# Kernel optimization log

Measured on AMD Instinct MI355X. Metric: run time of the kernel, lower is better.

## Reference

```python
import jax, jax.numpy as jnp
import numpy as np

D_E = 128
D_R = 128  # must equal D_E for the original torch code to typecheck
BN_EPS = 1e-5


def setup_inputs() -> dict:
    key = jax.random.key(0)
    ks = jax.random.split(key, 8)
    B, S = 16, 2048
    h = jax.random.normal(ks[0], (B, S, D_E), dtype=jnp.float32)
    r = jax.random.normal(ks[1], (B, S, D_R), dtype=jnp.float32)
    t = jax.random.normal(ks[2], (B, S, D_E), dtype=jnp.float32)
    # Xavier-uniform core tensor W: (d_r, d_e, d_e)
    limit = float(np.sqrt(6.0 / (D_R + D_E * D_E)))
    W = jax.random.uniform(ks[3], (D_R, D_E, D_E), minval=-limit, maxval=limit, dtype=jnp.float32)
    # BatchNorm1d params/buffers (inference mode)
    gamma0 = jnp.ones((D_E,), jnp.float32)
    beta0 = jnp.zeros((D_E,), jnp.float32)
    mean0 = 0.1 * jax.random.normal(ks[4], (D_E,), dtype=jnp.float32)
    var0 = jnp.abs(1.0 + 0.1 * jax.random.normal(ks[5], (D_E,), dtype=jnp.float32))
    gamma1 = jnp.ones((D_E,), jnp.float32)
    beta1 = jnp.zeros((D_E,), jnp.float32)
    mean1 = 0.1 * jax.random.normal(ks[6], (D_E,), dtype=jnp.float32)
    var1 = jnp.abs(1.0 + 0.1 * jax.random.normal(ks[7], (D_E,), dtype=jnp.float32))
    return {"h": h, "r": r, "t": t, "W": W,
            "gamma0": gamma0, "beta0": beta0, "mean0": mean0, "var0": var0,
            "gamma1": gamma1, "beta1": beta1, "mean1": mean1, "var1": var1}


def reference(h, r, t, W, gamma0, beta0, mean0, var0, gamma1, beta1, mean1, var1):
    B, S, D = h.shape  # D == d_e == d_r
    N = B * S
    # BatchNorm1d in eval mode over last dim; dropout is identity in eval.
    h_bn = (h - mean0) * jax.lax.rsqrt(var0 + BN_EPS) * gamma0 + beta0
    t_bn = (t - mean1) * jax.lax.rsqrt(var1 + BN_EPS) * gamma1 + beta1
    r2 = r.reshape(N, D)
    # torch.matmul((N,d_r), (d_r,d_e,d_e)) broadcasts -> shape (d_r, N, d_e):
    #   out[k, n, j] = sum_i r2[n, i] * W[k, i, j]
    # followed by .view(N, d_e, d_e) which reinterprets the flat buffer.
    W_mat = jnp.einsum('ni,kij->knj', r2, W).reshape(N, D, D)  # (N, d_e, d_e) after scrambled view
    # hr[n, j] = sum_d h_bn[n, d] * W_mat[n, d, j]
    hr = jnp.einsum('nd,ndj->nj', h_bn.reshape(N, D), W_mat)
    scores = jnp.sum(hr * t_bn.reshape(N, D), axis=-1)  # (N,)
    return scores.reshape(B, S)
```

## Files before the change

### kernel.cpp

```cpp
#include <hip/hip_runtime.h>


typedef __attribute__((ext_vector_type(8))) short bf16x8;
typedef __attribute__((ext_vector_type(4))) short s16x4;
typedef __attribute__((ext_vector_type(4))) float f32x4;

#define DPAD 136
#define BN_EPS 1e-5f

__device__ inline unsigned short f2bf(float f) {
  unsigned u = __builtin_bit_cast(unsigned, f);
  u += 0x7FFFu + ((u >> 16) & 1u);
  return (unsigned short)(u >> 16);
}
__device__ inline float bf2f(unsigned short h) {
  unsigned u = ((unsigned)h) << 16;
  return __builtin_bit_cast(float, u);
}
__device__ inline unsigned pack2bf(float lo, float hi) {
  return (unsigned)f2bf(lo) | ((unsigned)f2bf(hi) << 16);
}

__device__ inline int xcd_map(int bid) { return (bid & 7) * 64 + (bid >> 3); }

__global__ __launch_bounds__(256, 2) void k_stageA(
    const float* __restrict__ t, const float* __restrict__ W,
    const float* __restrict__ gamma1, const float* __restrict__ beta1,
    const float* __restrict__ mean1, const float* __restrict__ var1,
    unsigned short* __restrict__ V) {
  __shared__ short LA[64 * DPAD];
  __shared__ short LB[128 * DPAD];
  const int tid = threadIdx.x;
  const int c = tid & 31;
  const int rr = tid >> 5;
  const int wv_ = tid >> 6;
  const int lane = tid & 63;
  const int l16 = lane & 15;
  const int quad = lane >> 4;

  const int wg = xcd_map(blockIdx.x);
  const int k = wg >> 2;
  const int quarter = wg & 3;
  const int rowbase = k * 256 + quarter * 64;

  f32x4 g  = *(const f32x4*)(gamma1 + c * 4);
  f32x4 be = *(const f32x4*)(beta1  + c * 4);
  f32x4 mu = *(const f32x4*)(mean1  + c * 4);
  f32x4 va = *(const f32x4*)(var1   + c * 4);
  f32x4 sc, bi;
  for (int q = 0; q < 4; ++q) {
    sc[q] = g[q] * rsqrtf(va[q] + BN_EPS);
    bi[q] = be[q] - mu[q] * sc[q];
  }
  const float* tbase = t + (size_t)rowbase * 128;
  const float* wbase = W + (size_t)k * 16384;
#pragma unroll
  for (int it = 0; it < 8; ++it) {
    const int m = it * 8 + rr;
    f32x4 tv = *(const f32x4*)(tbase + m * 128 + c * 4);
    s16x4 tb;
    for (int q = 0; q < 4; ++q) tb[q] = (short)f2bf(tv[q] * sc[q] + bi[q]);
    *(s16x4*)(&LA[m * DPAD + c * 4]) = tb;
  }
#pragma unroll
  for (int it = 0; it < 16; ++it) {
    const int m = it * 8 + rr;
    f32x4 wvv = *(const f32x4*)(wbase + m * 128 + c * 4);
    s16x4 wb;
    for (int q = 0; q < 4; ++q) wb[q] = (short)f2bf(wvv[q]);
    *(s16x4*)(&LB[m * DPAD + c * 4]) = wb;
  }
  __syncthreads();

  f32x4 acc[8];
#pragma unroll
  for (int nt = 0; nt < 8; ++nt) acc[nt] = (f32x4){0.f, 0.f, 0.f, 0.f};

  __builtin_amdgcn_s_setprio(1);
#pragma unroll
  for (int ks = 0; ks < 4; ++ks) {
    const int K0 = ks * 32 + quad * 8;
    bf16x8 a = *(const bf16x8*)(&LA[(wv_ * 16 + l16) * DPAD + K0]);
    bf16x8 b[8];
#pragma unroll
    for (int nt = 0; nt < 8; ++nt)
      b[nt] = *(const bf16x8*)(&LB[(nt * 16 + l16) * DPAD + K0]);
#pragma unroll
    for (int nt = 0; nt < 8; ++nt)
      acc[nt] = __builtin_amdgcn_mfma_f32_16x16x32_bf16(b[nt], a, acc[nt], 0, 0, 0);
  }
  __builtin_amdgcn_s_setprio(0);

  const size_t np = (size_t)(rowbase + wv_ * 16 + l16) * 128;
#pragma unroll
  for (int nt = 0; nt < 8; ++nt) {
    unsigned two[2];
    two[0] = pack2bf(acc[nt][0], acc[nt][1]);
    two[1] = pack2bf(acc[nt][2], acc[nt][3]);
    *(uint2*)(V + np + nt * 16 + quad * 4) = *(uint2*)two;
  }
}

__global__ __launch_bounds__(256, 2) void k_bdot(
    const float* __restrict__ h, const float* __restrict__ r,
    const float* __restrict__ gamma0, const float* __restrict__ beta0,
    const float* __restrict__ mean0, const float* __restrict__ var0,
    const unsigned short* __restrict__ V, float* __restrict__ out) {
  __shared__ short LA[64 * DPAD];
  __shared__ short LB[128 * DPAD];
  const int tid = threadIdx.x;
  const int c = tid & 31;
  const int rr = tid >> 5;
  const int wv_ = tid >> 6;
  const int lane = tid & 63;
  const int l16 = lane & 15;
  const int quad = lane >> 4;

  const int wg = xcd_map(blockIdx.x);
  const int low = wg >> 1;
  const int half = wg & 1;
  const int kkbase = half * 64;

  f32x4 g  = *(const f32x4*)(gamma0 + c * 4);
  f32x4 be = *(const f32x4*)(beta0  + c * 4);
  f32x4 mu = *(const f32x4*)(mean0  + c * 4);
  f32x4 va = *(const f32x4*)(var0   + c * 4);
  f32x4 sc, bi;
  for (int q = 0; q < 4; ++q) {
    sc[q] = g[q] * rsqrtf(va[q] + BN_EPS);
    bi[q] = be[q] - mu[q] * sc[q];
  }
#pragma unroll
  for (int it = 0; it < 8; ++it) {
    const int kkloc = it * 8 + rr;
    f32x4 hv = *(const f32x4*)(h + ((size_t)(kkbase + kkloc) * 256 + low) * 128 + c * 4);
    s16x4 hb;
    for (int q = 0; q < 4; ++q) hb[q] = (short)f2bf(hv[q] * sc[q] + bi[q]);
    *(s16x4*)(&LA[kkloc * DPAD + c * 4]) = hb;
  }
#pragma unroll
  for (int it = 0; it < 4; ++it) {
    const int a0 = it * 32 + rr * 4;
    f32x4 rv[4];
    for (int v = 0; v < 4; ++v)
      rv[v] = *(const f32x4*)(r + ((size_t)(low * 128 + a0 + v)) * 128 + c * 4);
    for (int u = 0; u < 4; ++u) {
      s16x4 w;
      for (int v = 0; v < 4; ++v) w[v] = (short)f2bf(rv[v][u]);
      *(s16x4*)(&LB[(c * 4 + u) * DPAD + a0]) = w;
    }
  }
  __syncthreads();

  f32x4 acc[8];
#pragma unroll
  for (int nt = 0; nt < 8; ++nt) acc[nt] = (f32x4){0.f, 0.f, 0.f, 0.f};

  __builtin_amdgcn_s_setprio(1);
#pragma unroll
  for (int ks = 0; ks < 4; ++ks) {
    const int K0 = ks * 32 + quad * 8;
    bf16x8 a = *(const bf16x8*)(&LA[(wv_ * 16 + l16) * DPAD + K0]);
    bf16x8 b[8];
#pragma unroll
    for (int nt = 0; nt < 8; ++nt)
      b[nt] = *(const bf16x8*)(&LB[(nt * 16 + l16) * DPAD + K0]);
#pragma unroll
    for (int nt = 0; nt < 8; ++nt)
      acc[nt] = __builtin_amdgcn_mfma_f32_16x16x32_bf16(b[nt], a, acc[nt], 0, 0, 0);
  }
  __builtin_amdgcn_s_setprio(0);

  const int kk = kkbase + wv_ * 16 + l16;
  const size_t np = ((size_t)kk * 256 + low) * 128;
  float s = 0.f;
#pragma unroll
  for (int nt = 0; nt < 8; ++nt) {
    const uint2 vv = *(const uint2*)(V + np + nt * 16 + quad * 4);
    s += acc[nt][0] * bf2f((unsigned short)(vv.x & 0xFFFFu));
    s += acc[nt][1] * bf2f((unsigned short)(vv.x >> 16));
    s += acc[nt][2] * bf2f((unsigned short)(vv.y & 0xFFFFu));
    s += acc[nt][3] * bf2f((unsigned short)(vv.y >> 16));
  }
  s += __shfl_xor(s, 16, 64);
  s += __shfl_xor(s, 32, 64);
  if (quad == 0) out[(size_t)kk * 256 + low] = s;
}

extern "C" void kernel_launch(void* const* d_in, const int* in_sizes, int n_in,
                              void* d_out, int out_size, void* d_ws, size_t ws_size,
                              hipStream_t stream) {
  const float* h      = (const float*)d_in[0];
  const float* r      = (const float*)d_in[1];
  const float* t      = (const float*)d_in[2];
  const float* W      = (const float*)d_in[3];
  const float* gamma0 = (const float*)d_in[4];
  const float* beta0  = (const float*)d_in[5];
  const float* mean0  = (const float*)d_in[6];
  const float* var0   = (const float*)d_in[7];
  const float* gamma1 = (const float*)d_in[8];
  const float* beta1  = (const float*)d_in[9];
  const float* mean1  = (const float*)d_in[10];
  const float* var1   = (const float*)d_in[11];
  float* out = (float*)d_out;

  unsigned short* V = (unsigned short*)d_ws;

  k_stageA<<<512, 256, 0, stream>>>(t, W, gamma1, beta1, mean1, var1, V);
  k_bdot<<<512, 256, 0, stream>>>(h, r, gamma0, beta0, mean0, var0, V, out);
}
```

Baseline: 117.0 us.

## Fuse both stages into one cooperative kernel with per-block flag sync

Merges the stage-A GEMM and the bilinear-dot kernel into a single cooperatively launched kernel. Each block publishes a release flag once its V tile is written, then runs its second-stage GEMM and spins only on the 64 producer flags it needs before reading V. This removes the kernel boundary and lets the second stage's loads and MFMA overlap with producers still finishing. In exchange it adds a memset launch, cooperative launch overhead and spin-wait traffic, and it relies on all 512 blocks being co-resident.

```diff
diff --git a/kernel.cpp b/kernel.cpp
--- a/kernel.cpp
+++ b/kernel.cpp
@@ -23,11 +23,15 @@
 
 __device__ inline int xcd_map(int bid) { return (bid & 7) * 64 + (bid >> 3); }
 
-__global__ __launch_bounds__(256, 2) void k_stageA(
+__global__ __launch_bounds__(256, 2) void k_fused(
     const float* __restrict__ t, const float* __restrict__ W,
     const float* __restrict__ gamma1, const float* __restrict__ beta1,
     const float* __restrict__ mean1, const float* __restrict__ var1,
-    unsigned short* __restrict__ V) {
+    const float* __restrict__ h, const float* __restrict__ r,
+    const float* __restrict__ gamma0, const float* __restrict__ beta0,
+    const float* __restrict__ mean0, const float* __restrict__ var0,
+    unsigned short* __restrict__ V, unsigned* __restrict__ flags,
+    float* __restrict__ out) {
   __shared__ short LA[64 * DPAD];
   __shared__ short LB[128 * DPAD];
   const int tid = threadIdx.x;
@@ -39,152 +43,153 @@
   const int quad = lane >> 4;
 
   const int wg = xcd_map(blockIdx.x);
-  const int k = wg >> 2;
-  const int quarter = wg & 3;
-  const int rowbase = k * 256 + quarter * 64;
-
-  f32x4 g  = *(const f32x4*)(gamma1 + c * 4);
-  f32x4 be = *(const f32x4*)(beta1  + c * 4);
-  f32x4 mu = *(const f32x4*)(mean1  + c * 4);
-  f32x4 va = *(const f32x4*)(var1   + c * 4);
-  f32x4 sc, bi;
-  for (int q = 0; q < 4; ++q) {
-    sc[q] = g[q] * rsqrtf(va[q] + BN_EPS);
-    bi[q] = be[q] - mu[q] * sc[q];
+
+  {
+    const int k = wg >> 2;
+    const int quarter = wg & 3;
+    const int rowbase = k * 256 + quarter * 64;
+
+    f32x4 g  = *(const f32x4*)(gamma1 + c * 4);
+    f32x4 be = *(const f32x4*)(beta1  + c * 4);
+    f32x4 mu = *(const f32x4*)(mean1  + c * 4);
+    f32x4 va = *(const f32x4*)(var1   + c * 4);
+    f32x4 sc, bi;
+    for (int q = 0; q < 4; ++q) {
+      sc[q] = g[q] * rsqrtf(va[q] + BN_EPS);
+      bi[q] = be[q] - mu[q] * sc[q];
+    }
+    const float* tbase = t + (size_t)rowbase * 128;
+    const float* wbase = W + (size_t)k * 16384;
+#pragma unroll
+    for (int it = 0; it < 8; ++it) {
+      const int m = it * 8 + rr;
+      f32x4 tv = *(const f32x4*)(tbase + m * 128 + c * 4);
+      s16x4 tb;
+      for (int q = 0; q < 4; ++q) tb[q] = (short)f2bf(tv[q] * sc[q] + bi[q]);
+      *(s16x4*)(&LA[m * DPAD + c * 4]) = tb;
+    }
+#pragma unroll
+    for (int it = 0; it < 16; ++it) {
+      const int m = it * 8 + rr;
+      f32x4 wvv = *(const f32x4*)(wbase + m * 128 + c * 4);
+      s16x4 wb;
+      for (int q = 0; q < 4; ++q) wb[q] = (short)f2bf(wvv[q]);
+      *(s16x4*)(&LB[m * DPAD + c * 4]) = wb;
+    }
+    __syncthreads();
+
+    f32x4 acc[8];
+#pragma unroll
+    for (int nt = 0; nt < 8; ++nt) acc[nt] = (f32x4){0.f, 0.f, 0.f, 0.f};
+
+    __builtin_amdgcn_s_setprio(1);
+#pragma unroll
+    for (int ks = 0; ks < 4; ++ks) {
+      const int K0 = ks * 32 + quad * 8;
+      bf16x8 a = *(const bf16x8*)(&LA[(wv_ * 16 + l16) * DPAD + K0]);
+      bf16x8 b[8];
+#pragma unroll
+      for (int nt = 0; nt < 8; ++nt)
+        b[nt] = *(const bf16x8*)(&LB[(nt * 16 + l16) * DPAD + K0]);
+#pragma unroll
+      for (int nt = 0; nt < 8; ++nt)
+        acc[nt] = __builtin_amdgcn_mfma_f32_16x16x32_bf16(b[nt], a, acc[nt], 0, 0, 0);
+    }
+    __builtin_amdgcn_s_setprio(0);
+
+    const size_t np = (size_t)(rowbase + wv_ * 16 + l16) * 128;
+#pragma unroll
+    for (int nt = 0; nt < 8; ++nt) {
+      unsigned two[2];
+      two[0] = pack2bf(acc[nt][0], acc[nt][1]);
+      two[1] = pack2bf(acc[nt][2], acc[nt][3]);
+      *(uint2*)(V + np + nt * 16 + quad * 4) = *(uint2*)two;
+    }
   }
-  const float* tbase = t + (size_t)rowbase * 128;
-  const float* wbase = W + (size_t)k * 16384;
-#pragma unroll
-  for (int it = 0; it < 8; ++it) {
-    const int m = it * 8 + rr;
-    f32x4 tv = *(const f32x4*)(tbase + m * 128 + c * 4);
-    s16x4 tb;
-    for (int q = 0; q < 4; ++q) tb[q] = (short)f2bf(tv[q] * sc[q] + bi[q]);
-    *(s16x4*)(&LA[m * DPAD + c * 4]) = tb;
+
+  __syncthreads();
+  if (tid == 0)
+    __hip_atomic_store(&flags[wg], 1u, __ATOMIC_RELEASE, __HIP_MEMORY_SCOPE_AGENT);
+
+  {
+    const int low = wg >> 1;
+    const int half = wg & 1;
+    const int kkbase = half * 64;
+
+    f32x4 g  = *(const f32x4*)(gamma0 + c * 4);
+    f32x4 be = *(const f32x4*)(beta0  + c * 4);
+    f32x4 mu = *(const f32x4*)(mean0  + c * 4);
+    f32x4 va = *(const f32x4*)(var0   + c * 4);
+    f32x4 sc, bi;
+    for (int q = 0; q < 4; ++q) {
+      sc[q] = g[q] * rsqrtf(va[q] + BN_EPS);
+      bi[q] = be[q] - mu[q] * sc[q];
+    }
+#pragma unroll
+    for (int it = 0; it < 8; ++it) {
+      const int kkloc = it * 8 + rr;
+      f32x4 hv = *(const f32x4*)(h + ((size_t)(kkbase + kkloc) * 256 + low) * 128 + c * 4);
+      s16x4 hb;
+      for (int q = 0; q < 4; ++q) hb[q] = (short)f2bf(hv[q] * sc[q] + bi[q]);
+      *(s16x4*)(&LA[kkloc * DPAD + c * 4]) = hb;
+    }
+#pragma unroll
+    for (int it = 0; it < 4; ++it) {
+      const int a0 = it * 32 + rr * 4;
+      f32x4 rv[4];
+      for (int v = 0; v < 4; ++v)
+        rv[v] = *(const f32x4*)(r + ((size_t)(low * 128 + a0 + v)) * 128 + c * 4);
+      for (int u = 0; u < 4; ++u) {
+        s16x4 w;
+        for (int v = 0; v < 4; ++v) w[v] = (short)f2bf(rv[v][u]);
+        *(s16x4*)(&LB[(c * 4 + u) * DPAD + a0]) = w;
+      }
+    }
+    __syncthreads();
+
+    f32x4 acc[8];
+#pragma unroll
+    for (int nt = 0; nt < 8; ++nt) acc[nt] = (f32x4){0.f, 0.f, 0.f, 0.f};
+
+    __builtin_amdgcn_s_setprio(1);
+#pragma unroll
+    for (int ks = 0; ks < 4; ++ks) {
+      const int K0 = ks * 32 + quad * 8;
+      bf16x8 a = *(const bf16x8*)(&LA[(wv_ * 16 + l16) * DPAD + K0]);
+      bf16x8 b[8];
+#pragma unroll
+      for (int nt = 0; nt < 8; ++nt)
+        b[nt] = *(const bf16x8*)(&LB[(nt * 16 + l16) * DPAD + K0]);
+#pragma unroll
+      for (int nt = 0; nt < 8; ++nt)
+        acc[nt] = __builtin_amdgcn_mfma_f32_16x16x32_bf16(b[nt], a, acc[nt], 0, 0, 0);
+    }
+    __builtin_amdgcn_s_setprio(0);
+
+    if (tid < 64) {
+      const int pid = ((kkbase + tid) << 2) | (low >> 6);
+      while (__hip_atomic_load(&flags[pid], __ATOMIC_ACQUIRE,
+                               __HIP_MEMORY_SCOPE_AGENT) == 0u)
+        __builtin_amdgcn_s_sleep(2);
+    }
+    __syncthreads();
+    __builtin_amdgcn_fence(__ATOMIC_ACQUIRE, "agent");
+
+    const int kk = kkbase + wv_ * 16 + l16;
+    const size_t np = ((size_t)kk * 256 + low) * 128;
+    float s = 0.f;
+#pragma unroll
+    for (int nt = 0; nt < 8; ++nt) {
+      const uint2 vv = *(const uint2*)(V + np + nt * 16 + quad * 4);
+      s += acc[nt][0] * bf2f((unsigned short)(vv.x & 0xFFFFu));
+      s += acc[nt][1] * bf2f((unsigned short)(vv.x >> 16));
+      s += acc[nt][2] * bf2f((unsigned short)(vv.y & 0xFFFFu));
+      s += acc[nt][3] * bf2f((unsigned short)(vv.y >> 16));
+    }
+    s += __shfl_xor(s, 16, 64);
+    s += __shfl_xor(s, 32, 64);
+    if (quad == 0) out[(size_t)kk * 256 + low] = s;
   }
-#pragma unroll
-  for (int it = 0; it < 16; ++it) {
-    const int m = it * 8 + rr;
-    f32x4 wvv = *(const f32x4*)(wbase + m * 128 + c * 4);
-    s16x4 wb;
-    for (int q = 0; q < 4; ++q) wb[q] = (short)f2bf(wvv[q]);
-    *(s16x4*)(&LB[m * DPAD + c * 4]) = wb;
-  }
-  __syncthreads();
-
-  f32x4 acc[8];
-#pragma unroll
-  for (int nt = 0; nt < 8; ++nt) acc[nt] = (f32x4){0.f, 0.f, 0.f, 0.f};
-
-  __builtin_amdgcn_s_setprio(1);
-#pragma unroll
-  for (int ks = 0; ks < 4; ++ks) {
-    const int K0 = ks * 32 + quad * 8;
-    bf16x8 a = *(const bf16x8*)(&LA[(wv_ * 16 + l16) * DPAD + K0]);
-    bf16x8 b[8];
-#pragma unroll
-    for (int nt = 0; nt < 8; ++nt)
-      b[nt] = *(const bf16x8*)(&LB[(nt * 16 + l16) * DPAD + K0]);
-#pragma unroll
-    for (int nt = 0; nt < 8; ++nt)
-      acc[nt] = __builtin_amdgcn_mfma_f32_16x16x32_bf16(b[nt], a, acc[nt], 0, 0, 0);
-  }
-  __builtin_amdgcn_s_setprio(0);
-
-  const size_t np = (size_t)(rowbase + wv_ * 16 + l16) * 128;
-#pragma unroll
-  for (int nt = 0; nt < 8; ++nt) {
-    unsigned two[2];
-    two[0] = pack2bf(acc[nt][0], acc[nt][1]);
-    two[1] = pack2bf(acc[nt][2], acc[nt][3]);
-    *(uint2*)(V + np + nt * 16 + quad * 4) = *(uint2*)two;
-  }
-}
-
-__global__ __launch_bounds__(256, 2) void k_bdot(
-    const float* __restrict__ h, const float* __restrict__ r,
-    const float* __restrict__ gamma0, const float* __restrict__ beta0,
-    const float* __restrict__ mean0, const float* __restrict__ var0,
-    const unsigned short* __restrict__ V, float* __restrict__ out) {
-  __shared__ short LA[64 * DPAD];
-  __shared__ short LB[128 * DPAD];
-  const int tid = threadIdx.x;
-  const int c = tid & 31;
-  const int rr = tid >> 5;
-  const int wv_ = tid >> 6;
-  const int lane = tid & 63;
-  const int l16 = lane & 15;
-  const int quad = lane >> 4;
-
-  const int wg = xcd_map(blockIdx.x);
-  const int low = wg >> 1;
-  const int half = wg & 1;
-  const int kkbase = half * 64;
-
-  f32x4 g  = *(const f32x4*)(gamma0 + c * 4);
-  f32x4 be = *(const f32x4*)(beta0  + c * 4);
-  f32x4 mu = *(const f32x4*)(mean0  + c * 4);
-  f32x4 va = *(const f32x4*)(var0   + c * 4);
-  f32x4 sc, bi;
-  for (int q = 0; q < 4; ++q) {
-    sc[q] = g[q] * rsqrtf(va[q] + BN_EPS);
-    bi[q] = be[q] - mu[q] * sc[q];
-  }
-#pragma unroll
-  for (int it = 0; it < 8; ++it) {
-    const int kkloc = it * 8 + rr;
-    f32x4 hv = *(const f32x4*)(h + ((size_t)(kkbase + kkloc) * 256 + low) * 128 + c * 4);
-    s16x4 hb;
-    for (int q = 0; q < 4; ++q) hb[q] = (short)f2bf(hv[q] * sc[q] + bi[q]);
-    *(s16x4*)(&LA[kkloc * DPAD + c * 4]) = hb;
-  }
-#pragma unroll
-  for (int it = 0; it < 4; ++it) {
-    const int a0 = it * 32 + rr * 4;
-    f32x4 rv[4];
-    for (int v = 0; v < 4; ++v)
-      rv[v] = *(const f32x4*)(r + ((size_t)(low * 128 + a0 + v)) * 128 + c * 4);
-    for (int u = 0; u < 4; ++u) {
-      s16x4 w;
-      for (int v = 0; v < 4; ++v) w[v] = (short)f2bf(rv[v][u]);
-      *(s16x4*)(&LB[(c * 4 + u) * DPAD + a0]) = w;
-    }
-  }
-  __syncthreads();
-
-  f32x4 acc[8];
-#pragma unroll
-  for (int nt = 0; nt < 8; ++nt) acc[nt] = (f32x4){0.f, 0.f, 0.f, 0.f};
-
-  __builtin_amdgcn_s_setprio(1);
-#pragma unroll
-  for (int ks = 0; ks < 4; ++ks) {
-    const int K0 = ks * 32 + quad * 8;
-    bf16x8 a = *(const bf16x8*)(&LA[(wv_ * 16 + l16) * DPAD + K0]);
-    bf16x8 b[8];
-#pragma unroll
-    for (int nt = 0; nt < 8; ++nt)
-      b[nt] = *(const bf16x8*)(&LB[(nt * 16 + l16) * DPAD + K0]);
-#pragma unroll
-    for (int nt = 0; nt < 8; ++nt)
-      acc[nt] = __builtin_amdgcn_mfma_f32_16x16x32_bf16(b[nt], a, acc[nt], 0, 0, 0);
-  }
-  __builtin_amdgcn_s_setprio(0);
-
-  const int kk = kkbase + wv_ * 16 + l16;
-  const size_t np = ((size_t)kk * 256 + low) * 128;
-  float s = 0.f;
-#pragma unroll
-  for (int nt = 0; nt < 8; ++nt) {
-    const uint2 vv = *(const uint2*)(V + np + nt * 16 + quad * 4);
-    s += acc[nt][0] * bf2f((unsigned short)(vv.x & 0xFFFFu));
-    s += acc[nt][1] * bf2f((unsigned short)(vv.x >> 16));
-    s += acc[nt][2] * bf2f((unsigned short)(vv.y & 0xFFFFu));
-    s += acc[nt][3] * bf2f((unsigned short)(vv.y >> 16));
-  }
-  s += __shfl_xor(s, 16, 64);
-  s += __shfl_xor(s, 32, 64);
-  if (quad == 0) out[(size_t)kk * 256 + low] = s;
 }
 
 extern "C" void kernel_launch(void* const* d_in, const int* in_sizes, int n_in,
@@ -205,7 +210,14 @@
   float* out = (float*)d_out;
 
   unsigned short* V = (unsigned short*)d_ws;
-
-  k_stageA<<<512, 256, 0, stream>>>(t, W, gamma1, beta1, mean1, var1, V);
-  k_bdot<<<512, 256, 0, stream>>>(h, r, gamma0, beta0, mean0, var0, V, out);
-}
+  unsigned* flags = (unsigned*)((char*)d_ws + (size_t)32768 * 128 * 2);
+
+  hipMemsetAsync(flags, 0, 512 * sizeof(unsigned), stream);
+
+  void* args[] = {(void*)&t, (void*)&W, (void*)&gamma1, (void*)&beta1,
+                  (void*)&mean1, (void*)&var1, (void*)&h, (void*)&r,
+                  (void*)&gamma0, (void*)&beta0, (void*)&mean0, (void*)&var0,
+                  (void*)&V, (void*)&flags, (void*)&out};
+  hipLaunchCooperativeKernel((const void*)k_fused, dim3(512), dim3(256),
+                             args, 0, stream);
+}
```

Result: slower. 187.5 us (+60.2%).

## Drop LDS staging; feed MFMA operands directly from global memory in registers

Applied to the files above, without the earlier changes.

Both kernels stop staging operand tiles in shared memory behind a block barrier. Each wave now loads its own fragments straight from global memory into registers, converts them to bf16 and issues the MFMAs. The second kernel also swaps which operand is contracted: V becomes the MFMA register operand, and the batch-normalised h is applied in the epilogue dot product. This removes LDS traffic, the barrier and the occupancy cap, at the cost of redundant global reads of W and r across waves and less coalesced per-lane loads.

```diff
diff --git a/kernel.cpp b/kernel.cpp
--- a/kernel.cpp
+++ b/kernel.cpp
@@ -2,10 +2,8 @@
 
 
 typedef __attribute__((ext_vector_type(8))) short bf16x8;
-typedef __attribute__((ext_vector_type(4))) short s16x4;
 typedef __attribute__((ext_vector_type(4))) float f32x4;
 
-#define DPAD 136
 #define BN_EPS 1e-5f
 
 __device__ inline unsigned short f2bf(float f) {
@@ -13,85 +11,75 @@
   u += 0x7FFFu + ((u >> 16) & 1u);
   return (unsigned short)(u >> 16);
 }
-__device__ inline float bf2f(unsigned short h) {
-  unsigned u = ((unsigned)h) << 16;
-  return __builtin_bit_cast(float, u);
-}
 __device__ inline unsigned pack2bf(float lo, float hi) {
   return (unsigned)f2bf(lo) | ((unsigned)f2bf(hi) << 16);
+}
+__device__ inline bf16x8 cvt8(f32x4 lo, f32x4 hi) {
+  bf16x8 o;
+  o[0] = (short)f2bf(lo[0]); o[1] = (short)f2bf(lo[1]);
+  o[2] = (short)f2bf(lo[2]); o[3] = (short)f2bf(lo[3]);
+  o[4] = (short)f2bf(hi[0]); o[5] = (short)f2bf(hi[1]);
+  o[6] = (short)f2bf(hi[2]); o[7] = (short)f2bf(hi[3]);
+  return o;
 }
 
 __device__ inline int xcd_map(int bid) { return (bid & 7) * 64 + (bid >> 3); }
 
-__global__ __launch_bounds__(256, 2) void k_stageA(
+__global__ __launch_bounds__(256) void k_vA(
     const float* __restrict__ t, const float* __restrict__ W,
     const float* __restrict__ gamma1, const float* __restrict__ beta1,
     const float* __restrict__ mean1, const float* __restrict__ var1,
     unsigned short* __restrict__ V) {
-  __shared__ short LA[64 * DPAD];
-  __shared__ short LB[128 * DPAD];
   const int tid = threadIdx.x;
-  const int c = tid & 31;
-  const int rr = tid >> 5;
   const int wv_ = tid >> 6;
   const int lane = tid & 63;
   const int l16 = lane & 15;
   const int quad = lane >> 4;
 
-  const int wg = xcd_map(blockIdx.x);
-  const int k = wg >> 2;
-  const int quarter = wg & 3;
-  const int rowbase = k * 256 + quarter * 64;
+  const int w = xcd_map(blockIdx.x) * 4 + wv_;
+  const int k = w >> 4;
+  const int rg = w & 15;
+  const int nrow = k * 256 + rg * 16 + l16;
 
-  f32x4 g  = *(const f32x4*)(gamma1 + c * 4);
-  f32x4 be = *(const f32x4*)(beta1  + c * 4);
-  f32x4 mu = *(const f32x4*)(mean1  + c * 4);
-  f32x4 va = *(const f32x4*)(var1   + c * 4);
-  f32x4 sc, bi;
-  for (int q = 0; q < 4; ++q) {
-    sc[q] = g[q] * rsqrtf(va[q] + BN_EPS);
-    bi[q] = be[q] - mu[q] * sc[q];
+  const float* tp = t + (size_t)nrow * 128;
+  bf16x8 tf[4];
+#pragma unroll
+  for (int ks = 0; ks < 4; ++ks) {
+    const int K0 = ks * 32 + quad * 8;
+    f32x4 g0 = *(const f32x4*)(gamma1 + K0), g1 = *(const f32x4*)(gamma1 + K0 + 4);
+    f32x4 b0 = *(const f32x4*)(beta1  + K0), b1 = *(const f32x4*)(beta1  + K0 + 4);
+    f32x4 m0 = *(const f32x4*)(mean1  + K0), m1 = *(const f32x4*)(mean1  + K0 + 4);
+    f32x4 v0 = *(const f32x4*)(var1   + K0), v1 = *(const f32x4*)(var1   + K0 + 4);
+    f32x4 t0 = *(const f32x4*)(tp + K0),     t1 = *(const f32x4*)(tp + K0 + 4);
+    f32x4 lo, hi;
+    for (int q = 0; q < 4; ++q) {
+      const float s0 = g0[q] * rsqrtf(v0[q] + BN_EPS);
+      lo[q] = t0[q] * s0 + (b0[q] - m0[q] * s0);
+      const float s1 = g1[q] * rsqrtf(v1[q] + BN_EPS);
+      hi[q] = t1[q] * s1 + (b1[q] - m1[q] * s1);
+    }
+    tf[ks] = cvt8(lo, hi);
   }
-  const float* tbase = t + (size_t)rowbase * 128;
-  const float* wbase = W + (size_t)k * 16384;
-#pragma unroll
-  for (int it = 0; it < 8; ++it) {
-    const int m = it * 8 + rr;
-    f32x4 tv = *(const f32x4*)(tbase + m * 128 + c * 4);
-    s16x4 tb;
-    for (int q = 0; q < 4; ++q) tb[q] = (short)f2bf(tv[q] * sc[q] + bi[q]);
-    *(s16x4*)(&LA[m * DPAD + c * 4]) = tb;
-  }
-#pragma unroll
-  for (int it = 0; it < 16; ++it) {
-    const int m = it * 8 + rr;
-    f32x4 wvv = *(const f32x4*)(wbase + m * 128 + c * 4);
-    s16x4 wb;
-    for (int q = 0; q < 4; ++q) wb[q] = (short)f2bf(wvv[q]);
-    *(s16x4*)(&LB[m * DPAD + c * 4]) = wb;
-  }
-  __syncthreads();
+
+  const float* wp = W + (size_t)k * 16384 + (size_t)l16 * 128;
 
   f32x4 acc[8];
 #pragma unroll
   for (int nt = 0; nt < 8; ++nt) acc[nt] = (f32x4){0.f, 0.f, 0.f, 0.f};
 
-  __builtin_amdgcn_s_setprio(1);
 #pragma unroll
   for (int ks = 0; ks < 4; ++ks) {
     const int K0 = ks * 32 + quad * 8;
-    bf16x8 a = *(const bf16x8*)(&LA[(wv_ * 16 + l16) * DPAD + K0]);
-    bf16x8 b[8];
 #pragma unroll
-    for (int nt = 0; nt < 8; ++nt)
-      b[nt] = *(const bf16x8*)(&LB[(nt * 16 + l16) * DPAD + K0]);
-#pragma unroll
-    for (int nt = 0; nt < 8; ++nt)
-      acc[nt] = __builtin_amdgcn_mfma_f32_16x16x32_bf16(b[nt], a, acc[nt], 0, 0, 0);
+    for (int nt = 0; nt < 8; ++nt) {
+      f32x4 w0 = *(const f32x4*)(wp + nt * 2048 + K0);
+      f32x4 w1 = *(const f32x4*)(wp + nt * 2048 + K0 + 4);
+      acc[nt] = __builtin_amdgcn_mfma_f32_16x16x32_bf16(cvt8(w0, w1), tf[ks],
+                                                        acc[nt], 0, 0, 0);
+    }
   }
-  __builtin_amdgcn_s_setprio(0);
 
-  const size_t np = (size_t)(rowbase + wv_ * 16 + l16) * 128;
+  const size_t np = (size_t)nrow * 128;
 #pragma unroll
   for (int nt = 0; nt < 8; ++nt) {
     unsigned two[2];
@@ -101,90 +89,66 @@
   }
 }
 
-__global__ __launch_bounds__(256, 2) void k_bdot(
+__global__ __launch_bounds__(256) void k_B2(
     const float* __restrict__ h, const float* __restrict__ r,
     const float* __restrict__ gamma0, const float* __restrict__ beta0,
     const float* __restrict__ mean0, const float* __restrict__ var0,
     const unsigned short* __restrict__ V, float* __restrict__ out) {
-  __shared__ short LA[64 * DPAD];
-  __shared__ short LB[128 * DPAD];
   const int tid = threadIdx.x;
-  const int c = tid & 31;
-  const int rr = tid >> 5;
   const int wv_ = tid >> 6;
   const int lane = tid & 63;
   const int l16 = lane & 15;
   const int quad = lane >> 4;
 
-  const int wg = xcd_map(blockIdx.x);
-  const int low = wg >> 1;
-  const int half = wg & 1;
-  const int kkbase = half * 64;
+  const int w = xcd_map(blockIdx.x) * 4 + wv_;
+  const int low = w >> 3;
+  const int kg = w & 7;
+  const int kk = kg * 16 + l16;
+  const size_t nprow = (size_t)kk * 256 + low;
 
-  f32x4 g  = *(const f32x4*)(gamma0 + c * 4);
-  f32x4 be = *(const f32x4*)(beta0  + c * 4);
-  f32x4 mu = *(const f32x4*)(mean0  + c * 4);
-  f32x4 va = *(const f32x4*)(var0   + c * 4);
-  f32x4 sc, bi;
-  for (int q = 0; q < 4; ++q) {
-    sc[q] = g[q] * rsqrtf(va[q] + BN_EPS);
-    bi[q] = be[q] - mu[q] * sc[q];
-  }
+  const unsigned short* vp = V + nprow * 128;
+  bf16x8 vf[4];
 #pragma unroll
-  for (int it = 0; it < 8; ++it) {
-    const int kkloc = it * 8 + rr;
-    f32x4 hv = *(const f32x4*)(h + ((size_t)(kkbase + kkloc) * 256 + low) * 128 + c * 4);
-    s16x4 hb;
-    for (int q = 0; q < 4; ++q) hb[q] = (short)f2bf(hv[q] * sc[q] + bi[q]);
-    *(s16x4*)(&LA[kkloc * DPAD + c * 4]) = hb;
-  }
-#pragma unroll
-  for (int it = 0; it < 4; ++it) {
-    const int a0 = it * 32 + rr * 4;
-    f32x4 rv[4];
-    for (int v = 0; v < 4; ++v)
-      rv[v] = *(const f32x4*)(r + ((size_t)(low * 128 + a0 + v)) * 128 + c * 4);
-    for (int u = 0; u < 4; ++u) {
-      s16x4 w;
-      for (int v = 0; v < 4; ++v) w[v] = (short)f2bf(rv[v][u]);
-      *(s16x4*)(&LB[(c * 4 + u) * DPAD + a0]) = w;
-    }
-  }
-  __syncthreads();
+  for (int ks = 0; ks < 4; ++ks)
+    vf[ks] = *(const bf16x8*)(vp + ks * 32 + quad * 8);
+
+  const float* rp = r + ((size_t)low * 128 + l16) * 128;
 
   f32x4 acc[8];
 #pragma unroll
   for (int nt = 0; nt < 8; ++nt) acc[nt] = (f32x4){0.f, 0.f, 0.f, 0.f};
 
-  __builtin_amdgcn_s_setprio(1);
 #pragma unroll
   for (int ks = 0; ks < 4; ++ks) {
     const int K0 = ks * 32 + quad * 8;
-    bf16x8 a = *(const bf16x8*)(&LA[(wv_ * 16 + l16) * DPAD + K0]);
-    bf16x8 b[8];
 #pragma unroll
-    for (int nt = 0; nt < 8; ++nt)
-      b[nt] = *(const bf16x8*)(&LB[(nt * 16 + l16) * DPAD + K0]);
-#pragma unroll
-    for (int nt = 0; nt < 8; ++nt)
-      acc[nt] = __builtin_amdgcn_mfma_f32_16x16x32_bf16(b[nt], a, acc[nt], 0, 0, 0);
+    for (int nt = 0; nt < 8; ++nt) {
+      f32x4 r0 = *(const f32x4*)(rp + nt * 2048 + K0);
+      f32x4 r1 = *(const f32x4*)(rp + nt * 2048 + K0 + 4);
+      acc[nt] = __builtin_amdgcn_mfma_f32_16x16x32_bf16(cvt8(r0, r1), vf[ks],
+                                                        acc[nt], 0, 0, 0);
+    }
   }
-  __builtin_amdgcn_s_setprio(0);
 
-  const int kk = kkbase + wv_ * 16 + l16;
-  const size_t np = ((size_t)kk * 256 + low) * 128;
+  const float* hp = h + nprow * 128;
   float s = 0.f;
 #pragma unroll
   for (int nt = 0; nt < 8; ++nt) {
-    const uint2 vv = *(const uint2*)(V + np + nt * 16 + quad * 4);
-    s += acc[nt][0] * bf2f((unsigned short)(vv.x & 0xFFFFu));
-    s += acc[nt][1] * bf2f((unsigned short)(vv.x >> 16));
-    s += acc[nt][2] * bf2f((unsigned short)(vv.y & 0xFFFFu));
-    s += acc[nt][3] * bf2f((unsigned short)(vv.y >> 16));
+    const int a0 = nt * 16 + quad * 4;
+    f32x4 hv = *(const f32x4*)(hp + a0);
+    f32x4 g  = *(const f32x4*)(gamma0 + a0);
+    f32x4 be = *(const f32x4*)(beta0  + a0);
+    f32x4 mu = *(const f32x4*)(mean0  + a0);
+    f32x4 va = *(const f32x4*)(var0   + a0);
+    for (int q = 0; q < 4; ++q) {
+      const float sc = g[q] * rsqrtf(va[q] + BN_EPS);
+      const float hb = hv[q] * sc + (be[q] - mu[q] * sc);
+      s += hb * acc[nt][q];
+    }
   }
   s += __shfl_xor(s, 16, 64);
   s += __shfl_xor(s, 32, 64);
-  if (quad == 0) out[(size_t)kk * 256 + low] = s;
+  if (quad == 0) out[nprow] = s;
 }
 
 extern "C" void kernel_launch(void* const* d_in, const int* in_sizes, int n_in,
@@ -206,6 +170,6 @@
 
   unsigned short* V = (unsigned short*)d_ws;
 
-  k_stageA<<<512, 256, 0, stream>>>(t, W, gamma1, beta1, mean1, var1, V);
-  k_bdot<<<512, 256, 0, stream>>>(h, r, gamma0, beta0, mean0, var0, V, out);
+  k_vA<<<512, 256, 0, stream>>>(t, W, gamma1, beta1, mean1, var1, V);
+  k_B2<<<512, 256, 0, stream>>>(h, r, gamma0, beta0, mean0, var0, V, out);
 }
```

New measurement: 138.1 us. +18.0%, slower.
